# Kernel tuning notes

Hardware: AMD Instinct MI355X
Metric: run time of the kernel (lower is better)

Reference implementation:

```python
import jax, jax.numpy as jnp
import numpy as np


def _edt_one(mask):
    """Exact 2D Euclidean distance transform of one (H, W) binary map.

    Distance from each pixel to the nearest foreground (==1) pixel; 0 at
    foreground pixels (matches scipy-style distance_map_from_binary_matrix).
    Pass 1: 1D L1 distance along the width via forward/backward scans.
    Pass 2: exact lower-envelope min over rows (brute-force, vectorized).
    """
    H, W = mask.shape
    INF = jnp.float32(H + W)  # larger than any achievable distance
    g = jnp.where(mask > 0.5, jnp.float32(0.0), INF)  # (H, W)

    def step(carry, col):  # carry: (H,) running distance, col: (H,)
        d = jnp.minimum(col, carry + 1.0)
        return d, d

    init = jnp.full((H,), INF, dnp := jnp.float32)
    _, f = jax.lax.scan(step, init, g.T)           # (W, H) left-to-right
    _, b = jax.lax.scan(step, init, g.T[::-1])     # (W, H) right-to-left
    d1 = jnp.minimum(f, b[::-1]).T                 # (H, W) 1D distance along width

    ii = jnp.arange(H, dtype=jnp.float32)
    offs = (ii[:, None] - ii[None, :]) ** 2        # (H, H) squared row offsets
    # D2[i, j] = min_i' d1[i', j]^2 + (i - i')^2  -> intermediate (H, H, W)
    D2 = jnp.min(d1[None, :, :] ** 2 + offs[:, :, None], axis=1)
    return jnp.sqrt(D2)


def compute_distance_map(y_true):
    N, C, H, W = y_true.shape
    flat = y_true.reshape(N * C, H, W)
    dm = jax.lax.map(_edt_one, flat).reshape(N, C, H, W)  # sequential over N*C images
    return dm / jnp.float32(max(H, W) - 1)


def setup_inputs() -> dict:
    key = jax.random.key(0)
    k1, k2 = jax.random.split(key)
    y_pred = jax.random.normal(k1, (8, 2, 512, 512), dtype=jnp.float32)
    y_true = jax.random.randint(k2, (8, 2, 512, 512), 0, 2).astype(jnp.float32)
    return {"y_pred": y_pred, "y_true": y_true}


def reference(y_pred, y_true):
    # mode == 'multiclass', from_logits=True: log_softmax(dim=1).exp() == softmax
    p = jax.nn.softmax(y_pred, axis=1)
    sqe = (p - y_true) ** 2
    # torch version computes the map on CPU via numpy -> detached from autodiff
    dm = jax.lax.stop_gradient(compute_distance_map(y_true))
    loss = jnp.mean((1.0 + dm) * sqe, axis=(0, 2, 3))  # per-channel mean
    return loss.mean()
```

## Files before the change

kernel.cpp:

```cpp
#include <hip/hip_runtime.h>
#include <math.h>


#define H 512
#define W 512
#define NIMG 16
#define HW (H * W)
#define RW 5
#define SEG 16
#define WLEN (SEG + 2 * RW)

__global__ __launch_bounds__(256) void edt_rows_kernel(const float* __restrict__ yt,
                                                       float* __restrict__ d1sq) {
    int wid = blockIdx.x * 4 + (threadIdx.x >> 6);
    int lane = threadIdx.x & 63;
    int img = wid >> 9;
    int row = wid & (H - 1);

    const float* rp = yt + ((size_t)img * H + row) * W;
    int k0 = lane * 8;
    float4 va = *reinterpret_cast<const float4*>(rp + k0);
    float4 vb = *reinterpret_cast<const float4*>(rp + k0 + 4);
    float g[8] = { va.x, va.y, va.z, va.w, vb.x, vb.y, vb.z, vb.w };
    const float INF = 1024.0f;
    #pragma unroll
    for (int t = 0; t < 8; ++t) g[t] = (g[t] > 0.5f) ? 0.0f : INF;

    const float BIG = 3.0e38f;
    float pm[8], sm[8];

    float run = BIG;
    #pragma unroll
    for (int t = 0; t < 8; ++t) {
        float a = g[t] - (float)(k0 + t);
        run = fminf(run, a);
        pm[t] = run;
    }
    float incl = run;
    #pragma unroll
    for (int d = 1; d < 64; d <<= 1) {
        float o = __shfl_up(incl, d);
        if (lane >= d) incl = fminf(incl, o);
    }
    float excl = __shfl_up(incl, 1);
    if (lane == 0) excl = BIG;

    run = BIG;
    #pragma unroll
    for (int t = 7; t >= 0; --t) {
        float cc = g[t] + (float)(k0 + t);
        run = fminf(run, cc);
        sm[t] = run;
    }
    float incl2 = run;
    #pragma unroll
    for (int d = 1; d < 64; d <<= 1) {
        float o = __shfl_down(incl2, d);
        if (lane < 64 - d) incl2 = fminf(incl2, o);
    }
    float excl2 = __shfl_down(incl2, 1);
    if (lane == 63) excl2 = BIG;

    float out[8];
    #pragma unroll
    for (int t = 0; t < 8; ++t) {
        float kf = (float)(k0 + t);
        float f = kf + fminf(excl, pm[t]);
        float b = -kf + fminf(excl2, sm[t]);
        float d = fminf(f, b);
        out[t] = d * d;
    }
    float* op = d1sq + (size_t)img * HW + (size_t)row * W + k0;
    *reinterpret_cast<float4*>(op)     = make_float4(out[0], out[1], out[2], out[3]);
    *reinterpret_cast<float4*>(op + 4) = make_float4(out[4], out[5], out[6], out[7]);
}

__global__ __launch_bounds__(256) void edt_cols_loss_kernel(const float* __restrict__ yp,
                                                            const float* __restrict__ yt,
                                                            const float* __restrict__ d1sq,
                                                            double* __restrict__ part) {
    __shared__ double wsum[4];

    int jl  = threadIdx.x;
    int j   = blockIdx.x * 256 + jl;
    int i0  = blockIdx.y * SEG;
    int img = blockIdx.z;

    const float* dp = d1sq + (size_t)img * HW;
    const float BIG = 3.0e38f;

    float wsq[WLEN];
    #pragma unroll
    for (int k = 0; k < WLEN; ++k) {
        int ip = i0 - RW + k;
        if (ip >= 0 && ip < H) wsq[k] = dp[ip * W + j];
        else                   wsq[k] = BIG;
    }

    const float C2[2 * RW + 1] = {25.f,16.f,9.f,4.f,1.f,0.f,1.f,4.f,9.f,16.f,25.f};
    float mn[SEG];
    #pragma unroll
    for (int m = 0; m < SEG; ++m) {
        float v = wsq[m] + C2[0];
        #pragma unroll
        for (int k = 1; k < 2 * RW + 1; ++k)
            v = fminf(v, wsq[m + k] + C2[k]);
        mn[m] = v;
    }

    bool need = false;
    const float thr = (float)((RW + 1) * (RW + 1));
    #pragma unroll
    for (int m = 0; m < SEG; ++m) need |= (mn[m] > thr);
    if (__any(need)) {
        for (int ip = 0; ip < H; ++ip) {
            float w = dp[ip * W + j];
            #pragma unroll
            for (int m = 0; m < SEG; ++m) {
                int d = (i0 + m) - ip;
                mn[m] = fminf(mn[m], w + (float)(d * d));
            }
        }
    }

    int n = img >> 1;
    int c = img & 1;
    const float* ypc = yp + (size_t)(n * 2 + c) * HW;
    const float* ypo = yp + (size_t)(n * 2 + (1 - c)) * HW;
    const float* ytc = yt + (size_t)img * HW;

    double local = 0.0;
    #pragma unroll
    for (int m = 0; m < SEG; ++m) {
        int i = i0 + m;
        int idx = i * W + j;
        float dmv = sqrtf(mn[m]) / 511.0f;
        float x0 = ypc[idx], x1 = ypo[idx];
        float mx = fmaxf(x0, x1);
        float e0 = expf(x0 - mx), e1 = expf(x1 - mx);
        float p  = e0 / (e0 + e1);
        float df = p - ytc[idx];
        local += (double)((1.0f + dmv) * (df * df));
    }

    #pragma unroll
    for (int d = 32; d > 0; d >>= 1) local += __shfl_down(local, d);
    int wv = threadIdx.x >> 6;
    if ((threadIdx.x & 63) == 0) wsum[wv] = local;
    __syncthreads();
    if (threadIdx.x == 0) {
        double s = wsum[0] + wsum[1] + wsum[2] + wsum[3];
        part[((blockIdx.z * gridDim.y) + blockIdx.y) * gridDim.x + blockIdx.x] = s;
    }
}

__global__ __launch_bounds__(256) void finalize_kernel(const double* __restrict__ part,
                                                       float* __restrict__ out) {
    __shared__ double ws[4];
    int t = threadIdx.x;
    double v = part[t] + part[t + 256] + part[t + 512] + part[t + 768];
    #pragma unroll
    for (int d = 32; d > 0; d >>= 1) v += __shfl_down(v, d);
    if ((t & 63) == 0) ws[t >> 6] = v;
    __syncthreads();
    if (t == 0)
        out[0] = (float)((ws[0] + ws[1] + ws[2] + ws[3]) / (double)(NIMG * HW));
}

extern "C" void kernel_launch(void* const* d_in, const int* in_sizes, int n_in,
                              void* d_out, int out_size, void* d_ws, size_t ws_size,
                              hipStream_t stream) {
    const float* y_pred = (const float*)d_in[0];
    const float* y_true = (const float*)d_in[1];
    float* out = (float*)d_out;

    double* part = (double*)d_ws;
    float*  d1sq = (float*)((char*)d_ws + 16384);

    edt_rows_kernel<<<dim3(NIMG * H / 4), 256, 0, stream>>>(y_true, d1sq);
    edt_cols_loss_kernel<<<dim3(2, H / SEG, NIMG), 256, 0, stream>>>(y_pred, y_true, d1sq, part);
    finalize_kernel<<<1, 256, 0, stream>>>(part, out);
}
```

Baseline: 91.36 us.

## Fuse row EDT, column EDT, loss and finalize into one kernel

```diff
diff --git a/kernel.cpp b/kernel.cpp
--- a/kernel.cpp
+++ b/kernel.cpp
@@ -8,94 +8,96 @@
 #define HW (H * W)
 #define RW 5
 #define SEG 16
-#define WLEN (SEG + 2 * RW)
-
-__global__ __launch_bounds__(256) void edt_rows_kernel(const float* __restrict__ yt,
-                                                       float* __restrict__ d1sq) {
-    int wid = blockIdx.x * 4 + (threadIdx.x >> 6);
-    int lane = threadIdx.x & 63;
-    int img = wid >> 9;
-    int row = wid & (H - 1);
-
-    const float* rp = yt + ((size_t)img * H + row) * W;
-    int k0 = lane * 8;
-    float4 va = *reinterpret_cast<const float4*>(rp + k0);
-    float4 vb = *reinterpret_cast<const float4*>(rp + k0 + 4);
-    float g[8] = { va.x, va.y, va.z, va.w, vb.x, vb.y, vb.z, vb.w };
+#define HALO (SEG + 2*RW)
+#define NBLK (NIMG * (H / SEG))
+
+__global__ __launch_bounds__(512) void fused_loss_kernel(
+        const float* __restrict__ yp, const float* __restrict__ yt,
+        double* __restrict__ part, unsigned int* __restrict__ counter,
+        float* __restrict__ out) {
+    __shared__ float lw[HALO][W];
+    __shared__ double wsum[8];
+    __shared__ int fb;
+    __shared__ int lastf;
+
+    const int tid  = threadIdx.x;
+    const int wv   = tid >> 6;
+    const int lane = tid & 63;
+    const int img  = blockIdx.y;
+    const int i0   = blockIdx.x * SEG;
+    const int bid  = blockIdx.y * gridDim.x + blockIdx.x;
+
+    const float BIG = 3.0e38f;
     const float INF = 1024.0f;
-    #pragma unroll
-    for (int t = 0; t < 8; ++t) g[t] = (g[t] > 0.5f) ? 0.0f : INF;
-
-    const float BIG = 3.0e38f;
-    float pm[8], sm[8];
-
-    float run = BIG;
-    #pragma unroll
-    for (int t = 0; t < 8; ++t) {
-        float a = g[t] - (float)(k0 + t);
-        run = fminf(run, a);
-        pm[t] = run;
-    }
-    float incl = run;
-    #pragma unroll
-    for (int d = 1; d < 64; d <<= 1) {
-        float o = __shfl_up(incl, d);
-        if (lane >= d) incl = fminf(incl, o);
-    }
-    float excl = __shfl_up(incl, 1);
-    if (lane == 0) excl = BIG;
-
-    run = BIG;
-    #pragma unroll
-    for (int t = 7; t >= 0; --t) {
-        float cc = g[t] + (float)(k0 + t);
-        run = fminf(run, cc);
-        sm[t] = run;
-    }
-    float incl2 = run;
-    #pragma unroll
-    for (int d = 1; d < 64; d <<= 1) {
-        float o = __shfl_down(incl2, d);
-        if (lane < 64 - d) incl2 = fminf(incl2, o);
-    }
-    float excl2 = __shfl_down(incl2, 1);
-    if (lane == 63) excl2 = BIG;
-
-    float out[8];
-    #pragma unroll
-    for (int t = 0; t < 8; ++t) {
-        float kf = (float)(k0 + t);
-        float f = kf + fminf(excl, pm[t]);
-        float b = -kf + fminf(excl2, sm[t]);
-        float d = fminf(f, b);
-        out[t] = d * d;
-    }
-    float* op = d1sq + (size_t)img * HW + (size_t)row * W + k0;
-    *reinterpret_cast<float4*>(op)     = make_float4(out[0], out[1], out[2], out[3]);
-    *reinterpret_cast<float4*>(op + 4) = make_float4(out[4], out[5], out[6], out[7]);
-}
-
-__global__ __launch_bounds__(256) void edt_cols_loss_kernel(const float* __restrict__ yp,
-                                                            const float* __restrict__ yt,
-                                                            const float* __restrict__ d1sq,
-                                                            double* __restrict__ part) {
-    __shared__ double wsum[4];
-
-    int jl  = threadIdx.x;
-    int j   = blockIdx.x * 256 + jl;
-    int i0  = blockIdx.y * SEG;
-    int img = blockIdx.z;
-
-    const float* dp = d1sq + (size_t)img * HW;
-    const float BIG = 3.0e38f;
-
-    float wsq[WLEN];
-    #pragma unroll
-    for (int k = 0; k < WLEN; ++k) {
-        int ip = i0 - RW + k;
-        if (ip >= 0 && ip < H) wsq[k] = dp[ip * W + j];
-        else                   wsq[k] = BIG;
-    }
+    const float* ytimg = yt + (size_t)img * HW;
+
+    if (tid == 0) fb = 0;
+
+    for (int r = wv; r < HALO; r += 8) {
+        int ip = i0 - RW + r;
+        int k0 = lane * 8;
+        if (ip >= 0 && ip < H) {
+            const float* rp = ytimg + ip * W;
+            float4 va = *reinterpret_cast<const float4*>(rp + k0);
+            float4 vb = *reinterpret_cast<const float4*>(rp + k0 + 4);
+            float g[8] = { va.x, va.y, va.z, va.w, vb.x, vb.y, vb.z, vb.w };
+            #pragma unroll
+            for (int t = 0; t < 8; ++t) g[t] = (g[t] > 0.5f) ? 0.0f : INF;
+
+            float pm[8], sm[8];
+            float run = BIG;
+            #pragma unroll
+            for (int t = 0; t < 8; ++t) {
+                run = fminf(run, g[t] - (float)(k0 + t));
+                pm[t] = run;
+            }
+            float incl = run;
+            #pragma unroll
+            for (int d = 1; d < 64; d <<= 1) {
+                float o = __shfl_up(incl, d);
+                if (lane >= d) incl = fminf(incl, o);
+            }
+            float excl = __shfl_up(incl, 1);
+            if (lane == 0) excl = BIG;
+
+            run = BIG;
+            #pragma unroll
+            for (int t = 7; t >= 0; --t) {
+                run = fminf(run, g[t] + (float)(k0 + t));
+                sm[t] = run;
+            }
+            float incl2 = run;
+            #pragma unroll
+            for (int d = 1; d < 64; d <<= 1) {
+                float o = __shfl_down(incl2, d);
+                if (lane < 64 - d) incl2 = fminf(incl2, o);
+            }
+            float excl2 = __shfl_down(incl2, 1);
+            if (lane == 63) excl2 = BIG;
+
+            float o8[8];
+            #pragma unroll
+            for (int t = 0; t < 8; ++t) {
+                float kf = (float)(k0 + t);
+                float f = kf + fminf(excl, pm[t]);
+                float b = -kf + fminf(excl2, sm[t]);
+                float d = fminf(f, b);
+                o8[t] = d * d;
+            }
+            *reinterpret_cast<float4*>(&lw[r][k0])     = make_float4(o8[0], o8[1], o8[2], o8[3]);
+            *reinterpret_cast<float4*>(&lw[r][k0 + 4]) = make_float4(o8[4], o8[5], o8[6], o8[7]);
+        } else {
+            float4 b4 = make_float4(BIG, BIG, BIG, BIG);
+            *reinterpret_cast<float4*>(&lw[r][k0])     = b4;
+            *reinterpret_cast<float4*>(&lw[r][k0 + 4]) = b4;
+        }
+    }
+    __syncthreads();
+
+    const int j = tid;
+    float wsq[HALO];
+    #pragma unroll
+    for (int k = 0; k < HALO; ++k) wsq[k] = lw[k][j];
 
     const float C2[2 * RW + 1] = {25.f,16.f,9.f,4.f,1.f,0.f,1.f,4.f,9.f,16.f,25.f};
     float mn[SEG];
@@ -112,19 +114,75 @@
     const float thr = (float)((RW + 1) * (RW + 1));
     #pragma unroll
     for (int m = 0; m < SEG; ++m) need |= (mn[m] > thr);
-    if (__any(need)) {
-        for (int ip = 0; ip < H; ++ip) {
-            float w = dp[ip * W + j];
-            #pragma unroll
-            for (int m = 0; m < SEG; ++m) {
-                int d = (i0 + m) - ip;
-                mn[m] = fminf(mn[m], w + (float)(d * d));
+    if (__any(need) && lane == 0) atomicOr(&fb, 1);
+    __syncthreads();
+
+    if (fb) {
+        for (int base = 0; base < H; base += HALO) {
+            int rows = (H - base < HALO) ? (H - base) : HALO;
+            __syncthreads();
+            for (int r = wv; r < rows; r += 8) {
+                int ip = base + r;
+                int k0 = lane * 8;
+                const float* rp = ytimg + ip * W;
+                float4 va = *reinterpret_cast<const float4*>(rp + k0);
+                float4 vb = *reinterpret_cast<const float4*>(rp + k0 + 4);
+                float g[8] = { va.x, va.y, va.z, va.w, vb.x, vb.y, vb.z, vb.w };
+                #pragma unroll
+                for (int t = 0; t < 8; ++t) g[t] = (g[t] > 0.5f) ? 0.0f : INF;
+                float pm[8], sm[8];
+                float run = BIG;
+                #pragma unroll
+                for (int t = 0; t < 8; ++t) {
+                    run = fminf(run, g[t] - (float)(k0 + t));
+                    pm[t] = run;
+                }
+                float incl = run;
+                #pragma unroll
+                for (int d = 1; d < 64; d <<= 1) {
+                    float o = __shfl_up(incl, d);
+                    if (lane >= d) incl = fminf(incl, o);
+                }
+                float excl = __shfl_up(incl, 1);
+                if (lane == 0) excl = BIG;
+                run = BIG;
+                #pragma unroll
+                for (int t = 7; t >= 0; --t) {
+                    run = fminf(run, g[t] + (float)(k0 + t));
+                    sm[t] = run;
+                }
+                float incl2 = run;
+                #pragma unroll
+                for (int d = 1; d < 64; d <<= 1) {
+                    float o = __shfl_down(incl2, d);
+                    if (lane < 64 - d) incl2 = fminf(incl2, o);
+                }
+                float excl2 = __shfl_down(incl2, 1);
+                if (lane == 63) excl2 = BIG;
+                #pragma unroll
+                for (int t = 0; t < 8; ++t) {
+                    float kf = (float)(k0 + t);
+                    float f = kf + fminf(excl, pm[t]);
+                    float b = -kf + fminf(excl2, sm[t]);
+                    float d = fminf(f, b);
+                    lw[r][k0 + t] = d * d;
+                }
+            }
+            __syncthreads();
+            for (int k = 0; k < rows; ++k) {
+                int ip = base + k;
+                float w = lw[k][j];
+                #pragma unroll
+                for (int m = 0; m < SEG; ++m) {
+                    int d = (i0 + m) - ip;
+                    mn[m] = fminf(mn[m], w + (float)(d * d));
+                }
             }
         }
     }
 
-    int n = img >> 1;
-    int c = img & 1;
+    const int n = img >> 1;
+    const int c = img & 1;
     const float* ypc = yp + (size_t)(n * 2 + c) * HW;
     const float* ypo = yp + (size_t)(n * 2 + (1 - c)) * HW;
     const float* ytc = yt + (size_t)img * HW;
@@ -145,26 +203,34 @@
 
     #pragma unroll
     for (int d = 32; d > 0; d >>= 1) local += __shfl_down(local, d);
-    int wv = threadIdx.x >> 6;
-    if ((threadIdx.x & 63) == 0) wsum[wv] = local;
-    __syncthreads();
-    if (threadIdx.x == 0) {
-        double s = wsum[0] + wsum[1] + wsum[2] + wsum[3];
-        part[((blockIdx.z * gridDim.y) + blockIdx.y) * gridDim.x + blockIdx.x] = s;
-    }
-}
-
-__global__ __launch_bounds__(256) void finalize_kernel(const double* __restrict__ part,
-                                                       float* __restrict__ out) {
-    __shared__ double ws[4];
-    int t = threadIdx.x;
-    double v = part[t] + part[t + 256] + part[t + 512] + part[t + 768];
-    #pragma unroll
-    for (int d = 32; d > 0; d >>= 1) v += __shfl_down(v, d);
-    if ((t & 63) == 0) ws[t >> 6] = v;
-    __syncthreads();
-    if (t == 0)
-        out[0] = (float)((ws[0] + ws[1] + ws[2] + ws[3]) / (double)(NIMG * HW));
+    if (lane == 0) wsum[wv] = local;
+    __syncthreads();
+
+    if (tid == 0) {
+        double s = 0.0;
+        #pragma unroll
+        for (int q = 0; q < 8; ++q) s += wsum[q];
+        __hip_atomic_store(&part[bid], s, __ATOMIC_RELEASE, __HIP_MEMORY_SCOPE_AGENT);
+        unsigned int old = __hip_atomic_fetch_add(counter, 1u, __ATOMIC_ACQ_REL,
+                                                  __HIP_MEMORY_SCOPE_AGENT);
+        lastf = (old == NBLK - 1) ? 1 : 0;
+    }
+    __syncthreads();
+
+    if (lastf) {
+        double v = __hip_atomic_load(&part[tid], __ATOMIC_ACQUIRE,
+                                     __HIP_MEMORY_SCOPE_AGENT);
+        #pragma unroll
+        for (int d = 32; d > 0; d >>= 1) v += __shfl_down(v, d);
+        if (lane == 0) wsum[wv] = v;
+        __syncthreads();
+        if (tid == 0) {
+            double s = 0.0;
+            #pragma unroll
+            for (int q = 0; q < 8; ++q) s += wsum[q];
+            out[0] = (float)(s / (double)(NIMG * HW));
+        }
+    }
 }
 
 extern "C" void kernel_launch(void* const* d_in, const int* in_sizes, int n_in,
@@ -174,10 +240,10 @@
     const float* y_true = (const float*)d_in[1];
     float* out = (float*)d_out;
 
-    double* part = (double*)d_ws;
-    float*  d1sq = (float*)((char*)d_ws + 16384);
-
-    edt_rows_kernel<<<dim3(NIMG * H / 4), 256, 0, stream>>>(y_true, d1sq);
-    edt_cols_loss_kernel<<<dim3(2, H / SEG, NIMG), 256, 0, stream>>>(y_pred, y_true, d1sq, part);
-    finalize_kernel<<<1, 256, 0, stream>>>(part, out);
+    unsigned int* counter = (unsigned int*)d_ws;
+    double* part = (double*)((char*)d_ws + 4096);
+
+    hipMemsetAsync(d_ws, 0, 4, stream);
+    fused_loss_kernel<<<dim3(H / SEG, NIMG), 512, 0, stream>>>(
+        y_pred, y_true, part, counter, out);
 }
```

After: 98.73 us. 8.1% more time.

## Fold finalize into column kernel via last-block reduction, halve row segment, faster softmax

Applied to the files above, without the earlier changes.

```diff
diff --git a/kernel.cpp b/kernel.cpp
--- a/kernel.cpp
+++ b/kernel.cpp
@@ -7,11 +7,31 @@
 #define NIMG 16
 #define HW (H * W)
 #define RW 5
-#define SEG 16
-#define WLEN (SEG + 2 * RW)
+#define SEG 8
+#define HALO (SEG + 2 * RW)
+#define JT 256
+#define NBLK (NIMG * (H / SEG) * (W / JT))
+
+static __device__ __forceinline__ float fast_exp2(float x) {
+#if __has_builtin(__builtin_amdgcn_exp2f)
+    return __builtin_amdgcn_exp2f(x);
+#else
+    return exp2f(x);
+#endif
+}
+static __device__ __forceinline__ float fast_rcp(float x) {
+#if __has_builtin(__builtin_amdgcn_rcpf)
+    return __builtin_amdgcn_rcpf(x);
+#else
+    return 1.0f / x;
+#endif
+}
 
 __global__ __launch_bounds__(256) void edt_rows_kernel(const float* __restrict__ yt,
-                                                       float* __restrict__ d1sq) {
+                                                       float* __restrict__ d1sq,
+                                                       unsigned int* __restrict__ counter) {
+    if (blockIdx.x == 0 && threadIdx.x == 0) *counter = 0u;
+
     int wid = blockIdx.x * 4 + (threadIdx.x >> 6);
     int lane = threadIdx.x & 63;
     int img = wid >> 9;
@@ -32,8 +52,7 @@
     float run = BIG;
     #pragma unroll
     for (int t = 0; t < 8; ++t) {
-        float a = g[t] - (float)(k0 + t);
-        run = fminf(run, a);
+        run = fminf(run, g[t] - (float)(k0 + t));
         pm[t] = run;
     }
     float incl = run;
@@ -48,8 +67,7 @@
     run = BIG;
     #pragma unroll
     for (int t = 7; t >= 0; --t) {
-        float cc = g[t] + (float)(k0 + t);
-        run = fminf(run, cc);
+        run = fminf(run, g[t] + (float)(k0 + t));
         sm[t] = run;
     }
     float incl2 = run;
@@ -75,96 +93,100 @@
     *reinterpret_cast<float4*>(op + 4) = make_float4(out[4], out[5], out[6], out[7]);
 }
 
-__global__ __launch_bounds__(256) void edt_cols_loss_kernel(const float* __restrict__ yp,
-                                                            const float* __restrict__ yt,
-                                                            const float* __restrict__ d1sq,
-                                                            double* __restrict__ part) {
+__global__ __launch_bounds__(256) void edt_cols_loss_kernel(
+        const float* __restrict__ yp, const float* __restrict__ yt,
+        const float* __restrict__ d1sq, double* __restrict__ part,
+        unsigned int* __restrict__ counter, float* __restrict__ out) {
     __shared__ double wsum[4];
-
-    int jl  = threadIdx.x;
-    int j   = blockIdx.x * 256 + jl;
-    int i0  = blockIdx.y * SEG;
-    int img = blockIdx.z;
-
+    __shared__ int lastf;
+
+    const int tid  = threadIdx.x;
+    const int lane = tid & 63;
+    const int wv   = tid >> 6;
+    const int j    = blockIdx.x * JT + tid;
+    const int i0   = blockIdx.y * SEG;
+    const int img  = blockIdx.z;
+    const int bid  = (blockIdx.z * gridDim.y + blockIdx.y) * gridDim.x + blockIdx.x;
+
+    const float BIG = 3.0e38f;
     const float* dp = d1sq + (size_t)img * HW;
-    const float BIG = 3.0e38f;
-
-    float wsq[WLEN];
-    #pragma unroll
-    for (int k = 0; k < WLEN; ++k) {
+
+    float w[HALO];
+    #pragma unroll
+    for (int k = 0; k < HALO; ++k) {
         int ip = i0 - RW + k;
-        if (ip >= 0 && ip < H) wsq[k] = dp[ip * W + j];
-        else                   wsq[k] = BIG;
-    }
-
-    const float C2[2 * RW + 1] = {25.f,16.f,9.f,4.f,1.f,0.f,1.f,4.f,9.f,16.f,25.f};
+        w[k] = (ip >= 0 && ip < H) ? dp[ip * W + j] : BIG;
+    }
+
     float mn[SEG];
     #pragma unroll
     for (int m = 0; m < SEG; ++m) {
-        float v = wsq[m] + C2[0];
-        #pragma unroll
-        for (int k = 1; k < 2 * RW + 1; ++k)
-            v = fminf(v, wsq[m + k] + C2[k]);
-        mn[m] = v;
+        float a1 = fminf(w[m + 4], w[m + 6]) + 1.0f;
+        float a2 = fminf(w[m + 3], w[m + 7]) + 4.0f;
+        float a3 = fminf(w[m + 2], w[m + 8]) + 9.0f;
+        float a4 = fminf(w[m + 1], w[m + 9]) + 16.0f;
+        float a5 = fminf(w[m + 0], w[m + 10]) + 25.0f;
+        mn[m] = fminf(fminf(fminf(w[m + 5], a1), fminf(a2, a3)), fminf(a4, a5));
     }
 
     bool need = false;
-    const float thr = (float)((RW + 1) * (RW + 1));
-    #pragma unroll
-    for (int m = 0; m < SEG; ++m) need |= (mn[m] > thr);
+    #pragma unroll
+    for (int m = 0; m < SEG; ++m) need |= (mn[m] > 36.0f);
     if (__any(need)) {
         for (int ip = 0; ip < H; ++ip) {
-            float w = dp[ip * W + j];
+            float v = dp[ip * W + j];
             #pragma unroll
             for (int m = 0; m < SEG; ++m) {
                 int d = (i0 + m) - ip;
-                mn[m] = fminf(mn[m], w + (float)(d * d));
+                mn[m] = fminf(mn[m], v + (float)(d * d));
             }
         }
     }
 
-    int n = img >> 1;
-    int c = img & 1;
+    const int n = img >> 1;
+    const int c = img & 1;
     const float* ypc = yp + (size_t)(n * 2 + c) * HW;
     const float* ypo = yp + (size_t)(n * 2 + (1 - c)) * HW;
     const float* ytc = yt + (size_t)img * HW;
+    const float LOG2E = 1.44269504088896340736f;
 
     double local = 0.0;
     #pragma unroll
     for (int m = 0; m < SEG; ++m) {
-        int i = i0 + m;
-        int idx = i * W + j;
-        float dmv = sqrtf(mn[m]) / 511.0f;
-        float x0 = ypc[idx], x1 = ypo[idx];
-        float mx = fmaxf(x0, x1);
-        float e0 = expf(x0 - mx), e1 = expf(x1 - mx);
-        float p  = e0 / (e0 + e1);
+        int idx = (i0 + m) * W + j;
+        float dmv = sqrtf(mn[m]) * (1.0f / 511.0f);
+        float d  = ypo[idx] - ypc[idx];
+        float e  = fast_exp2(d * LOG2E);
+        float p  = fast_rcp(1.0f + e);
         float df = p - ytc[idx];
         local += (double)((1.0f + dmv) * (df * df));
     }
 
     #pragma unroll
     for (int d = 32; d > 0; d >>= 1) local += __shfl_down(local, d);
-    int wv = threadIdx.x >> 6;
-    if ((threadIdx.x & 63) == 0) wsum[wv] = local;
+    if (lane == 0) wsum[wv] = local;
     __syncthreads();
-    if (threadIdx.x == 0) {
+
+    if (tid == 0) {
         double s = wsum[0] + wsum[1] + wsum[2] + wsum[3];
-        part[((blockIdx.z * gridDim.y) + blockIdx.y) * gridDim.x + blockIdx.x] = s;
-    }
-}
-
-__global__ __launch_bounds__(256) void finalize_kernel(const double* __restrict__ part,
-                                                       float* __restrict__ out) {
-    __shared__ double ws[4];
-    int t = threadIdx.x;
-    double v = part[t] + part[t + 256] + part[t + 512] + part[t + 768];
-    #pragma unroll
-    for (int d = 32; d > 0; d >>= 1) v += __shfl_down(v, d);
-    if ((t & 63) == 0) ws[t >> 6] = v;
+        __hip_atomic_store(&part[bid], s, __ATOMIC_RELEASE, __HIP_MEMORY_SCOPE_AGENT);
+        unsigned int old = __hip_atomic_fetch_add(counter, 1u, __ATOMIC_ACQ_REL,
+                                                  __HIP_MEMORY_SCOPE_AGENT);
+        lastf = (old == NBLK - 1) ? 1 : 0;
+    }
     __syncthreads();
-    if (t == 0)
-        out[0] = (float)((ws[0] + ws[1] + ws[2] + ws[3]) / (double)(NIMG * HW));
+
+    if (lastf) {
+        double v = 0.0;
+        for (int q = tid; q < NBLK; q += 256)
+            v += __hip_atomic_load(&part[q], __ATOMIC_ACQUIRE, __HIP_MEMORY_SCOPE_AGENT);
+        #pragma unroll
+        for (int d = 32; d > 0; d >>= 1) v += __shfl_down(v, d);
+        if (lane == 0) wsum[wv] = v;
+        __syncthreads();
+        if (tid == 0)
+            out[0] = (float)((wsum[0] + wsum[1] + wsum[2] + wsum[3]) / (double)(NIMG * HW));
+    }
 }
 
 extern "C" void kernel_launch(void* const* d_in, const int* in_sizes, int n_in,
@@ -174,10 +196,11 @@
     const float* y_true = (const float*)d_in[1];
     float* out = (float*)d_out;
 
-    double* part = (double*)d_ws;
-    float*  d1sq = (float*)((char*)d_ws + 16384);
-
-    edt_rows_kernel<<<dim3(NIMG * H / 4), 256, 0, stream>>>(y_true, d1sq);
-    edt_cols_loss_kernel<<<dim3(2, H / SEG, NIMG), 256, 0, stream>>>(y_pred, y_true, d1sq, part);
-    finalize_kernel<<<1, 256, 0, stream>>>(part, out);
-}
+    unsigned int* counter = (unsigned int*)d_ws;
+    double* part = (double*)((char*)d_ws + 4096);
+    float*  d1sq = (float*)((char*)d_ws + 32768);
+
+    edt_rows_kernel<<<dim3(NIMG * H / 4), 256, 0, stream>>>(y_true, d1sq, counter);
+    edt_cols_loss_kernel<<<dim3(W / JT, H / SEG, NIMG), 256, 0, stream>>>(
+        y_pred, y_true, d1sq, part, counter, out);
+}
```

New measurement: 169.3 us. 85.3% more time.
